# Kernel optimization log

Measured on AMD Instinct MI355X. Metric: run time of the kernel, lower is better.

## Reference

```python
import math
import jax, jax.numpy as jnp
import numpy as np

EMB_DIM, EMB_KS, EMB_HS = 64, 2, 1
H, CS = 4, 32  # n_heads, GLA chunk size
EPS = 1e-5


def _ln4d(x, g, b):
    # LayerNormalization4D: normalize over channel dim (axis 1), biased var
    mu = x.mean(1, keepdims=True)
    var = ((x - mu) ** 2).mean(1, keepdims=True)
    return (x - mu) / jnp.sqrt(var + EPS) * g + b


def _unfold(x):
    # x [N,C,Q] -> [N, L, C*ks]; torch F.unfold feature order is c-major, k-minor
    N, C, Q = x.shape
    L = (Q - EMB_KS) // EMB_HS + 1
    f = jnp.stack([x[:, :, k:k + L] for k in range(EMB_KS)], axis=2)  # [N,C,ks,L]
    return f.reshape(N, C * EMB_KS, L).transpose(0, 2, 1)


def _deconv1d(x, w, b):
    # ConvTranspose1d, stride=EMB_HS=1; x [N,Cin,L], w [Cin,Cout,K]
    N, Cin, L = x.shape
    Cout, K = w.shape[1], w.shape[2]
    out_len = (L - 1) * EMB_HS + K
    y = jnp.zeros((N, Cout, out_len), x.dtype)
    for k in range(K):
        y = y.at[:, :, k:k + L].add(jnp.einsum('ncl,co->nol', x, w[:, :, k]))
    return y + b[None, :, None]


def _gla(x, Wq, Wk, Wv, Wg1, Wg2, Wr, gn, Wo):
    # chunked gated linear attention (use_gk=True, use_gv=False, swish output gate)
    N, L, D = x.shape
    Dk = Wq.shape[1] // H
    Dv = Wv.shape[1] // H
    Lp = -(-L // CS) * CS
    pad = Lp - L
    nc = Lp // CS
    q = (x @ Wq) * (Dk ** -0.5)
    k = x @ Wk
    v = x @ Wv
    gk = jax.nn.log_sigmoid((x @ Wg1) @ Wg2) / 32.0  # gate_logit_normalizer=32

    def chunk(t, dh):
        t = jnp.pad(t, ((0, 0), (0, pad), (0, 0)))
        return t.reshape(N, nc, CS, H, dh)

    q, k, gk, v = chunk(q, Dk), chunk(k, Dk), chunk(gk, Dk), chunk(v, Dv)
    gc = jnp.cumsum(gk, axis=2)                      # within-chunk log-decay [N,nc,CS,H,Dk]
    q_i = q * jnp.exp(gc)
    k_i = k * jnp.exp(-gc)
    mask = jnp.tril(jnp.ones((CS, CS), bool))
    A = jnp.einsum('ncthd,ncshd->nchts', q_i, k_i)   # intra-chunk scores
    A = jnp.where(mask[None, None, None], A, 0.0)
    o_intra = jnp.einsum('nchts,ncshd->ncthd', A, v)
    gl = gc[:, :, -1]                                 # chunk-total log decay [N,nc,H,Dk]
    k_o = k * jnp.exp(gl[:, :, None] - gc)

    def step(S, inp):
        qi, ko, vc, g = inp
        o = jnp.einsum('nthk,nhkv->nthv', qi, S)      # inter-chunk contribution
        S = S * jnp.exp(g)[..., None] + jnp.einsum('nthk,nthv->nhkv', ko, vc)
        return S, o

    S0 = jnp.zeros((N, H, Dk, Dv), x.dtype)
    xs = tuple(jnp.moveaxis(t, 1, 0) for t in (q_i, k_o, v, gl))
    _, o_inter = jax.lax.scan(step, S0, xs)
    o = (o_intra + jnp.moveaxis(o_inter, 0, 1)).reshape(N, Lp, H, Dv)[:, :L]
    # per-head RMSNorm + swish output gate
    o = o / jnp.sqrt(jnp.mean(o * o, -1, keepdims=True) + EPS) * gn.reshape(H, Dv)
    r = x @ Wr
    o = o.reshape(N, L, H * Dv) * (r * jax.nn.sigmoid(r))
    return o @ Wo


def _forward(x, mouth, intra_gamma, intra_beta, intra_Wq, intra_Wk, intra_Wv,
             intra_Wg1, intra_Wg2, intra_Wr, intra_gn, intra_Wo, intra_ct_w, intra_ct_b,
             inter_gamma, inter_beta, inter_Wq, inter_Wk, inter_Wv,
             inter_Wg1, inter_Wg2, inter_Wr, inter_gn, inter_Wo, inter_ct_w, inter_ct_b):
    B, C, old_T, old_Q = x.shape
    T = math.ceil((old_T - EMB_KS) / EMB_HS) * EMB_HS + EMB_KS
    Q = math.ceil((old_Q - EMB_KS) / EMB_HS) * EMB_HS + EMB_KS
    x = jnp.pad(x, ((0, 0), (0, 0), (0, T - old_T), (0, Q - old_Q)))
    # intra (frequency) path
    u = _ln4d(x, intra_gamma, intra_beta)
    u = u.transpose(0, 2, 1, 3).reshape(B * T, C, Q)
    f = _unfold(u)                                    # [B*T, Q-1, C*ks]
    g = _gla(f, intra_Wq, intra_Wk, intra_Wv, intra_Wg1, intra_Wg2, intra_Wr, intra_gn, intra_Wo)
    y = _deconv1d(g.transpose(0, 2, 1), intra_ct_w, intra_ct_b)  # [B*T, C, Q]
    y = y.reshape(B, T, C, Q).transpose(0, 2, 1, 3) + x
    # inter (time) path
    u = _ln4d(y, inter_gamma, inter_beta)
    u = u.transpose(0, 3, 1, 2).reshape(B * Q, C, T)
    f = _unfold(u)                                    # [B*Q, T-1, C*ks]
    g = _gla(f, inter_Wq, inter_Wk, inter_Wv, inter_Wg1, inter_Wg2, inter_Wr, inter_gn, inter_Wo)
    z = _deconv1d(g.transpose(0, 2, 1), inter_ct_w, inter_ct_b)  # [B*Q, C, T]
    z = z.reshape(B, Q, C, T).transpose(0, 2, 3, 1) + y
    return z[..., :old_T, :old_Q]


def setup_inputs() -> dict:
    key = jax.random.key(0)
    ks = jax.random.split(key, 32)
    D = EMB_DIM * EMB_KS       # 128 = GLA d_model
    DKV = 2 * D                # 256 (expand_k = expand_v = 2)

    def w(i, shape, fan):
        return jax.random.normal(ks[i], shape, jnp.float32) / np.sqrt(fan).astype(np.float32)

    inp = {
        'x': jax.random.normal(ks[0], (4, EMB_DIM, 256, 128), jnp.float32),
        'mouth': jax.random.normal(ks[1], (4, 1, 64, 64), jnp.float32),
    }
    for p, base in (('intra', 2), ('inter', 14)):
        inp[p + '_gamma'] = jnp.ones((1, EMB_DIM, 1, 1), jnp.float32)
        inp[p + '_beta'] = jnp.zeros((1, EMB_DIM, 1, 1), jnp.float32)
        inp[p + '_Wq'] = w(base, (D, DKV), D)
        inp[p + '_Wk'] = w(base + 1, (D, DKV), D)
        inp[p + '_Wv'] = w(base + 2, (D, DKV), D)
        inp[p + '_Wg1'] = w(base + 3, (D, 32), D)
        inp[p + '_Wg2'] = w(base + 4, (32, DKV), 32)
        inp[p + '_Wr'] = w(base + 5, (D, DKV), D)
        inp[p + '_gn'] = jnp.ones((DKV,), jnp.float32)
        inp[p + '_Wo'] = w(base + 6, (DKV, D), DKV)
        inp[p + '_ct_w'] = w(base + 7, (D, EMB_DIM, EMB_KS), D * EMB_KS)
        inp[p + '_ct_b'] = jnp.zeros((EMB_DIM,), jnp.float32)
    return inp


def reference(x, mouth, intra_gamma, intra_beta, intra_Wq, intra_Wk, intra_Wv,
              intra_Wg1, intra_Wg2, intra_Wr, intra_gn, intra_Wo, intra_ct_w, intra_ct_b,
              inter_gamma, inter_beta, inter_Wq, inter_Wk, inter_Wv,
              inter_Wg1, inter_Wg2, inter_Wr, inter_gn, inter_Wo, inter_ct_w, inter_ct_b):
    return _forward(x, mouth, intra_gamma, intra_beta, intra_Wq, intra_Wk, intra_Wv,
                    intra_Wg1, intra_Wg2, intra_Wr, intra_gn, intra_Wo, intra_ct_w, intra_ct_b,
                    inter_gamma, inter_beta, inter_Wq, inter_Wk, inter_Wv,
                    inter_Wg1, inter_Wg2, inter_Wr, inter_gn, inter_Wo, inter_ct_w, inter_ct_b)
```

## Files before the change

### kernel.cpp

```cpp
#include <hip/hip_runtime.h>

#define EPS 1e-5f

__device__ __forceinline__ float logsig(float z) {
    return fminf(z, 0.0f) - log1pf(__expf(-fabsf(z)));
}

template<int SLEN, int PSTRIDE>
__global__ __launch_bounds__(512)
__attribute__((amdgpu_waves_per_eu(2, 2)))
void gla_pass(const float* __restrict__ src, float* __restrict__ out,
              const float* __restrict__ gamma, const float* __restrict__ beta,
              const float* __restrict__ Wq, const float* __restrict__ Wk,
              const float* __restrict__ Wv, const float* __restrict__ Wg1,
              const float* __restrict__ Wg2, const float* __restrict__ Wr,
              const float* __restrict__ gn, const float* __restrict__ Wo,
              const float* __restrict__ ctw, const float* __restrict__ ctb)
{
    constexpr int NC = SLEN / 32;
    constexpr int L  = SLEN - 1;

    __shared__ __align__(16) float sxA[64][36];
    __shared__ __align__(16) float sxB[64][36];
    __shared__ __align__(16) float sxr[64][32];
    __shared__ __align__(16) float qf[32][256];
    __shared__ __align__(16) float kf[32][256];
    __shared__ __align__(16) float voc[32][256];
    __shared__ __align__(16) float uni[4608];
    __shared__ __align__(16) float fw1t[32][36];
    __shared__ __align__(16) float gprevs[128];
    __shared__ float egl[256];
    __shared__ float sgam[64], sbet[64];
    __shared__ float smu[33], sinv[33];
    __shared__ float gcarry[256];

    float* const Ats  = uni;
    float* const gdec = uni;

    const int tid  = threadIdx.x;
    const int lane = tid & 63;
    const int wv   = tid >> 6;
    const int h    = wv & 3;
    const int kh   = wv >> 2;
    const int d    = tid & 255;
    const int th   = (tid >> 8) & 1;
    const int n    = blockIdx.x;

    int b, fixedoff;
    if constexpr (PSTRIDE == 1) { b = n >> 8; fixedoff = (n & 255) * 128; }
    else                        { b = n >> 7; fixedoff = (n & 127); }
    const int cbase = (b * 64) * 32768 + fixedoff;

    if (tid < 64)  { sgam[tid] = gamma[tid]; sbet[tid] = beta[tid]; }
    if (tid < 128) gprevs[tid] = 0.0f;

    float S[32];
    #pragma unroll
    for (int k = 0; k < 32; ++k) S[k] = 0.0f;

    const float gnv  = gn[h * 64 + lane];
    const float bias = ctb[lane];

    #pragma unroll
    for (int k = 0; k < 5; ++k) {
        int idx = tid + k * 512;
        if (idx < 64 * 33) {
            int cc = idx / 33, i = idx - cc * 33;
            sxA[cc][i] = src[cbase + cc * 32768 + i * PSTRIDE];
        }
    }

    for (int ch = 0; ch < NC; ++ch) {
        const int l0 = ch * 32;
        float (* const cur)[36] = (ch & 1) ? sxB : sxA;
        float (* const nxt)[36] = (ch & 1) ? sxA : sxB;
        __syncthreads();

        float pre[5];
        const bool pf = (ch + 1 < NC);
        if (pf) {
            const int l0n = l0 + 32;
            #pragma unroll
            for (int k = 0; k < 5; ++k) {
                int idx = tid + k * 512;
                if (idx < 64 * 33) {
                    int cc = idx / 33, i = idx - cc * 33;
                    int p  = l0n + i; if (p > SLEN - 1) p = SLEN - 1;
                    pre[k] = src[cbase + cc * 32768 + p * PSTRIDE];
                }
            }
        }

        for (int col = wv; col < 33; col += 8) {
            float x = cur[lane][col];
            float s1 = x, s2 = x * x;
            #pragma unroll
            for (int off = 32; off > 0; off >>= 1) {
                s1 += __shfl_xor(s1, off, 64);
                s2 += __shfl_xor(s2, off, 64);
            }
            if (lane == 0) {
                float mu  = s1 * (1.0f / 64.0f);
                float var = s2 * (1.0f / 64.0f) - mu * mu;
                smu[col]  = mu;
                sinv[col] = rsqrtf(fmaxf(var, 0.0f) + EPS);
            }
        }
        __syncthreads();

        #pragma unroll
        for (int k = 0; k < 5; ++k) {
            int idx = tid + k * 512;
            if (idx < 64 * 33) {
                int cc = idx / 33, i = idx - cc * 33;
                float x = cur[cc][i];
                if (i < 32) sxr[cc][i] = x;
                cur[cc][i] = (x - smu[i]) * sinv[i] * sgam[cc] + sbet[cc];
            }
        }
        __syncthreads();

        {
            const int m = tid & 31, tg2 = tid >> 5;
            float a0 = 0.0f, a1 = 0.0f;
            for (int cc = 0; cc < 64; ++cc) {
                const float w0 = Wg1[(2*cc)*32 + m], w1 = Wg1[(2*cc+1)*32 + m];
                a0 += cur[cc][tg2]      * w0 + cur[cc][tg2 + 1]  * w1;
                a1 += cur[cc][tg2 + 16] * w0 + cur[cc][tg2 + 17] * w1;
            }
            fw1t[m][tg2] = a0; fw1t[m][tg2 + 16] = a1;
        }
        __syncthreads();

        float erunp[16], erunm[16];
        {
            const int t0 = th * 16;
            float acc2[16];
            #pragma unroll
            for (int t = 0; t < 16; ++t) acc2[t] = 0.0f;
            for (int mm = 0; mm < 32; ++mm) {
                const float w = Wg2[mm * 256 + d];
                #pragma unroll
                for (int i = 0; i < 4; ++i) {
                    float4 f4 = *(const float4*)&fw1t[mm][t0 + 4 * i];
                    acc2[4*i+0] += f4.x * w; acc2[4*i+1] += f4.y * w;
                    acc2[4*i+2] += f4.z * w; acc2[4*i+3] += f4.w * w;
                }
            }
            float r = 0.0f;
            #pragma unroll
            for (int t = 0; t < 16; ++t) {
                if ((l0 + t0 + t) < L) r += logsig(acc2[t]) * (1.0f / 32.0f);
                acc2[t] = r;
            }
            if (th == 0) gcarry[d] = r;
            __syncthreads();
            const float c = (th == 0) ? 0.0f : gcarry[d];
            #pragma unroll
            for (int t = 0; t < 16; ++t) {
                float run = c + acc2[t];
                erunp[t] = __expf(run);
                erunm[t] = __expf(-run);
            }
            if (th == 1) egl[d] = erunp[15];
        }

        if (pf) {
            #pragma unroll
            for (int k = 0; k < 5; ++k) {
                int idx = tid + k * 512;
                if (idx < 64 * 33) {
                    int cc = idx / 33, i = idx - cc * 33;
                    nxt[cc][i] = pre[k];
                }
            }
        }

        {
            const int t0 = th * 16;
            float aq[16], ak[16];
            #pragma unroll
            for (int t = 0; t < 16; ++t) { aq[t] = 0.0f; ak[t] = 0.0f; }
            for (int cc = 0; cc < 64; ++cc) {
                float col[17];
                #pragma unroll
                for (int i = 0; i < 4; ++i) {
                    float4 c4 = *(const float4*)&cur[cc][t0 + 4 * i];
                    col[4*i] = c4.x; col[4*i+1] = c4.y; col[4*i+2] = c4.z; col[4*i+3] = c4.w;
                }
                col[16] = cur[cc][t0 + 16];
                const float wq0 = Wq[(2*cc)*256 + d], wq1 = Wq[(2*cc+1)*256 + d];
                const float wk0 = Wk[(2*cc)*256 + d], wk1 = Wk[(2*cc+1)*256 + d];
                #pragma unroll
                for (int t = 0; t < 16; ++t) {
                    aq[t] += col[t] * wq0 + col[t+1] * wq1;
                    ak[t] += col[t] * wk0 + col[t+1] * wk1;
                }
            }
            #pragma unroll
            for (int t = 0; t < 16; ++t) {
                bool valid = (l0 + t0 + t) < L;
                qf[t0 + t][d] = valid ? aq[t] * 0.125f * erunp[t] : 0.0f;
                kf[t0 + t][d] = valid ? ak[t] * erunm[t] : 0.0f;
            }
        }
        {
            const int t0 = th * 16;
            float av[16];
            #pragma unroll
            for (int t = 0; t < 16; ++t) av[t] = 0.0f;
            for (int cc = 0; cc < 64; ++cc) {
                float col[17];
                #pragma unroll
                for (int i = 0; i < 4; ++i) {
                    float4 c4 = *(const float4*)&cur[cc][t0 + 4 * i];
                    col[4*i] = c4.x; col[4*i+1] = c4.y; col[4*i+2] = c4.z; col[4*i+3] = c4.w;
                }
                col[16] = cur[cc][t0 + 16];
                const float wv0 = Wv[(2*cc)*256 + d], wv1 = Wv[(2*cc+1)*256 + d];
                #pragma unroll
                for (int t = 0; t < 16; ++t) av[t] += col[t] * wv0 + col[t+1] * wv1;
            }
            #pragma unroll
            for (int t = 0; t < 16; ++t)
                voc[t0 + t][d] = ((l0 + t0 + t) < L) ? av[t] : 0.0f;
        }
        __syncthreads();

        const int base = h * 64;
        float vcol[32];
        #pragma unroll
        for (int t = 0; t < 32; ++t) vcol[t] = voc[t][base + lane];

        for (int pi = lane + 64 * kh; pi < 528; pi += 128) {
            float fpi = (float)pi;
            int t = (int)((sqrtf(8.0f * fpi + 1.0f) - 1.0f) * 0.5f);
            if (((t + 1) * (t + 2)) / 2 <= pi) ++t;
            if ((t * (t + 1)) / 2 > pi) --t;
            int s = pi - (t * (t + 1)) / 2;
            float a = 0.0f;
            #pragma unroll
            for (int ii = 0; ii < 16; ++ii) {
                int i = (ii + lane) & 15;
                float4 q4 = *(const float4*)&qf[t][base + 4 * i];
                float4 k4 = *(const float4*)&kf[s][base + 4 * i];
                a += q4.x*k4.x + q4.y*k4.y + q4.z*k4.z + q4.w*k4.w;
            }
            Ats[h * 1152 + t * 36 + s] = a;
        }
        __syncthreads();

        if (kh == 1) {
            #pragma unroll
            for (int t = 0; t < 32; ++t) {
                float oe = 0.0f;
                #pragma unroll
                for (int i = 0; i < 8; ++i) {
                    float4 q4 = *(const float4*)&qf[t][base + 32 + 4 * i];
                    oe += q4.x*S[4*i] + q4.y*S[4*i+1] + q4.z*S[4*i+2] + q4.w*S[4*i+3];
                }
                voc[t][base + lane] = oe;
            }
        }
        __syncthreads();

        if (kh == 0) {
            #pragma unroll
            for (int t = 0; t < 32; ++t) {
                float ot = voc[t][base + lane];
                #pragma unroll
                for (int i = 0; i < 8; ++i) {
                    float4 q4 = *(const float4*)&qf[t][base + 4 * i];
                    ot += q4.x*S[4*i] + q4.y*S[4*i+1] + q4.z*S[4*i+2] + q4.w*S[4*i+3];
                }
                const float* arow = &Ats[h * 1152 + t * 36];
                #pragma unroll
                for (int s4 = 0; s4 + 4 <= t + 1; s4 += 4) {
                    float4 a4 = *(const float4*)&arow[s4];
                    ot += a4.x*vcol[s4] + a4.y*vcol[s4+1] + a4.z*vcol[s4+2] + a4.w*vcol[s4+3];
                }
                #pragma unroll
                for (int s = (t + 1) & ~3; s <= t; ++s) ot += arow[s] * vcol[s];
                float ss = ot * ot;
                #pragma unroll
                for (int off = 32; off > 0; off >>= 1) ss += __shfl_xor(ss, off, 64);
                voc[t][base + lane] = ot * rsqrtf(ss * (1.0f / 64.0f) + EPS) * gnv;
            }
        } else {
            const int kb = base + 32;
            #pragma unroll
            for (int i = 0; i < 8; ++i) {
                float s0 = 0.0f, s1 = 0.0f, s2 = 0.0f, s3 = 0.0f;
                #pragma unroll
                for (int t = 0; t < 32; ++t) {
                    float4 k4 = *(const float4*)&kf[t][kb + 4 * i];
                    const float vt = vcol[t];
                    s0 += k4.x * vt; s1 += k4.y * vt; s2 += k4.z * vt; s3 += k4.w * vt;
                }
                S[4*i+0] = egl[kb + 4*i+0] * (S[4*i+0] + s0);
                S[4*i+1] = egl[kb + 4*i+1] * (S[4*i+1] + s1);
                S[4*i+2] = egl[kb + 4*i+2] * (S[4*i+2] + s2);
                S[4*i+3] = egl[kb + 4*i+3] * (S[4*i+3] + s3);
            }
        }
        __syncthreads();

        if (kh == 0) {
            const int kb = base;
            #pragma unroll
            for (int i = 0; i < 8; ++i) {
                float s0 = 0.0f, s1 = 0.0f, s2 = 0.0f, s3 = 0.0f;
                #pragma unroll
                for (int t = 0; t < 32; ++t) {
                    float4 k4 = *(const float4*)&kf[t][kb + 4 * i];
                    const float vt = vcol[t];
                    s0 += k4.x * vt; s1 += k4.y * vt; s2 += k4.z * vt; s3 += k4.w * vt;
                }
                S[4*i+0] = egl[kb + 4*i+0] * (S[4*i+0] + s0);
                S[4*i+1] = egl[kb + 4*i+1] * (S[4*i+1] + s1);
                S[4*i+2] = egl[kb + 4*i+2] * (S[4*i+2] + s2);
                S[4*i+3] = egl[kb + 4*i+3] * (S[4*i+3] + s3);
            }
        }

        {
            const int t0 = th * 16;
            float ar[16];
            #pragma unroll
            for (int t = 0; t < 16; ++t) ar[t] = 0.0f;
            for (int cc = 0; cc < 64; ++cc) {
                float col[17];
                #pragma unroll
                for (int i = 0; i < 4; ++i) {
                    float4 c4 = *(const float4*)&cur[cc][t0 + 4 * i];
                    col[4*i] = c4.x; col[4*i+1] = c4.y; col[4*i+2] = c4.z; col[4*i+3] = c4.w;
                }
                col[16] = cur[cc][t0 + 16];
                const float w0 = Wr[(2*cc)*256 + d], w1 = Wr[(2*cc+1)*256 + d];
                #pragma unroll
                for (int t = 0; t < 16; ++t) ar[t] += col[t] * w0 + col[t+1] * w1;
            }
            #pragma unroll
            for (int t = 0; t < 16; ++t) {
                const float r = ar[t];
                voc[t0 + t][d] *= r / (1.0f + __expf(-r));
            }
        }
        __syncthreads();

        {
            const int m2  = tid & 63;
            const int tg4 = tid >> 6;
            float accA[4] = {0,0,0,0}, accB[4] = {0,0,0,0};
            for (int j = 0; j < 256; j += 4) {
                float wA0 = Wo[(j+0)*128 + m2],      wB0 = Wo[(j+0)*128 + m2 + 64];
                float wA1 = Wo[(j+1)*128 + m2],      wB1 = Wo[(j+1)*128 + m2 + 64];
                float wA2 = Wo[(j+2)*128 + m2],      wB2 = Wo[(j+2)*128 + m2 + 64];
                float wA3 = Wo[(j+3)*128 + m2],      wB3 = Wo[(j+3)*128 + m2 + 64];
                #pragma unroll
                for (int i = 0; i < 4; ++i) {
                    float4 o4 = *(const float4*)&voc[tg4 * 4 + i][j];
                    accA[i] += o4.x*wA0 + o4.y*wA1 + o4.z*wA2 + o4.w*wA3;
                    accB[i] += o4.x*wB0 + o4.y*wB1 + o4.z*wB2 + o4.w*wB3;
                }
            }
            #pragma unroll
            for (int i = 0; i < 4; ++i) {
                gdec[(tg4 * 4 + i) * 132 + m2]      = accA[i];
                gdec[(tg4 * 4 + i) * 132 + m2 + 64] = accB[i];
            }
        }
        __syncthreads();

        {
            const int o  = lane;
            const int pg = wv;
            const float2* ctw2 = (const float2*)ctw;
            float acc4[4] = {0,0,0,0};
            for (int c4 = 0; c4 < 128; c4 += 4) {
                float2 w0 = ctw2[(c4+0)*64 + o];
                float2 w1 = ctw2[(c4+1)*64 + o];
                float2 w2 = ctw2[(c4+2)*64 + o];
                float2 w3 = ctw2[(c4+3)*64 + o];
                float4 r[5];
                r[0] = (pg == 0) ? *(const float4*)&gprevs[c4]
                                 : *(const float4*)&gdec[(pg*4 - 1) * 132 + c4];
                #pragma unroll
                for (int j = 0; j < 4; ++j)
                    r[j+1] = *(const float4*)&gdec[(pg*4 + j) * 132 + c4];
                #pragma unroll
                for (int i = 0; i < 4; ++i) {
                    acc4[i] += r[i+1].x*w0.x + r[i].x*w0.y
                             + r[i+1].y*w1.x + r[i].y*w1.y
                             + r[i+1].z*w2.x + r[i].z*w2.y
                             + r[i+1].w*w3.x + r[i].w*w3.y;
                }
            }
            #pragma unroll
            for (int i = 0; i < 4; ++i) {
                const int tl = pg * 4 + i;
                const int oi = cbase + o * 32768 + (l0 + tl) * PSTRIDE;
                out[oi] = acc4[i] + bias + sxr[o][tl];
            }
        }
        __syncthreads();
        if (tid < 128) gprevs[tid] = gdec[31 * 132 + tid];
    }
}

extern "C" void kernel_launch(void* const* d_in, const int* in_sizes, int n_in,
                              void* d_out, int out_size, void* d_ws, size_t ws_size,
                              hipStream_t stream)
{
    const float* x = (const float*)d_in[0];
    float* y = (float*)d_ws;
    float* z = (float*)d_out;

    gla_pass<128, 1><<<dim3(1024), dim3(512), 0, stream>>>(
        x, y,
        (const float*)d_in[2],  (const float*)d_in[3],  (const float*)d_in[4],
        (const float*)d_in[5],  (const float*)d_in[6],  (const float*)d_in[7],
        (const float*)d_in[8],  (const float*)d_in[9],  (const float*)d_in[10],
        (const float*)d_in[11], (const float*)d_in[12], (const float*)d_in[13]);

    gla_pass<256, 128><<<dim3(512), dim3(512), 0, stream>>>(
        y, z,
        (const float*)d_in[14], (const float*)d_in[15], (const float*)d_in[16],
        (const float*)d_in[17], (const float*)d_in[18], (const float*)d_in[19],
        (const float*)d_in[20], (const float*)d_in[21], (const float*)d_in[22],
        (const float*)d_in[23], (const float*)d_in[24], (const float*)d_in[25]);
}
```

Before: 5.909 ms.

## Pack projection weights into interleaved float4 layout and prefetch per iteration

Adds a small pre-kernel that repacks Wq/Wk, Wv/Wr and Wg1 into interleaved float4/float2 arrays in workspace, so each projection loop loads one vector per channel pair instead of four scalar loads, and software-prefetches the next iteration's weights. It also recomputes exp gates on the fly instead of holding 32 registers of exponentials to reduce register pressure, and halves the LayerNorm shuffle reduction by having each half-wave handle a column. Costs an extra launch plus workspace traffic each call, and Wv/Wr loads now fetch unused halves.

```diff
diff --git a/kernel.cpp b/kernel.cpp
--- a/kernel.cpp
+++ b/kernel.cpp
@@ -4,6 +4,43 @@
 
 __device__ __forceinline__ float logsig(float z) {
     return fminf(z, 0.0f) - log1pf(__expf(-fabsf(z)));
+}
+
+__global__ __launch_bounds__(256)
+void pack_weights(const float* __restrict__ Wq0, const float* __restrict__ Wk0,
+                  const float* __restrict__ Wv0, const float* __restrict__ Wr0,
+                  const float* __restrict__ Wg10,
+                  const float* __restrict__ Wq1, const float* __restrict__ Wk1,
+                  const float* __restrict__ Wv1, const float* __restrict__ Wr1,
+                  const float* __restrict__ Wg11,
+                  float* __restrict__ pk)
+{
+    int idx = blockIdx.x * 256 + threadIdx.x;
+    int p   = (idx >= 34816) ? 1 : 0;
+    int j   = idx - p * 34816;
+    const float* Wq  = p ? Wq1  : Wq0;
+    const float* Wk  = p ? Wk1  : Wk0;
+    const float* Wv  = p ? Wv1  : Wv0;
+    const float* Wr  = p ? Wr1  : Wr0;
+    const float* Wg1 = p ? Wg11 : Wg10;
+    float* base = pk + p * 135168;
+    if (j < 16384) {
+        int cc = j >> 8, d = j & 255;
+        float4 v = { Wq[(2*cc)*256 + d], Wq[(2*cc+1)*256 + d],
+                     Wk[(2*cc)*256 + d], Wk[(2*cc+1)*256 + d] };
+        ((float4*)base)[j] = v;
+    } else if (j < 32768) {
+        int jj = j - 16384;
+        int cc = jj >> 8, d = jj & 255;
+        float4 v = { Wv[(2*cc)*256 + d], Wv[(2*cc+1)*256 + d],
+                     Wr[(2*cc)*256 + d], Wr[(2*cc+1)*256 + d] };
+        ((float4*)(base + 65536))[jj] = v;
+    } else {
+        int jj = j - 32768;
+        int cc = jj >> 5, m = jj & 31;
+        float2 v = { Wg1[(2*cc)*32 + m], Wg1[(2*cc+1)*32 + m] };
+        ((float2*)(base + 131072))[jj] = v;
+    }
 }
 
 template<int SLEN, int PSTRIDE>
@@ -11,9 +48,9 @@
 __attribute__((amdgpu_waves_per_eu(2, 2)))
 void gla_pass(const float* __restrict__ src, float* __restrict__ out,
               const float* __restrict__ gamma, const float* __restrict__ beta,
-              const float* __restrict__ Wq, const float* __restrict__ Wk,
-              const float* __restrict__ Wv, const float* __restrict__ Wg1,
-              const float* __restrict__ Wg2, const float* __restrict__ Wr,
+              const float4* __restrict__ pWqk, const float4* __restrict__ pWvr,
+              const float2* __restrict__ pWg1,
+              const float* __restrict__ Wg2,
               const float* __restrict__ gn, const float* __restrict__ Wo,
               const float* __restrict__ ctw, const float* __restrict__ ctb)
 {
@@ -91,15 +128,20 @@
             }
         }
 
-        for (int col = wv; col < 33; col += 8) {
-            float x = cur[lane][col];
-            float s1 = x, s2 = x * x;
-            #pragma unroll
-            for (int off = 32; off > 0; off >>= 1) {
+        for (int cp = wv; cp < 17; cp += 8) {
+            const int col = 2 * cp + (lane >> 5);
+            float s1 = 0.0f, s2 = 0.0f;
+            if (col < 33) {
+                const int c0 = (lane & 31) * 2;
+                float x0 = cur[c0][col], x1 = cur[c0 + 1][col];
+                s1 = x0 + x1; s2 = x0 * x0 + x1 * x1;
+            }
+            #pragma unroll
+            for (int off = 16; off > 0; off >>= 1) {
                 s1 += __shfl_xor(s1, off, 64);
                 s2 += __shfl_xor(s2, off, 64);
             }
-            if (lane == 0) {
+            if ((lane & 31) == 0 && col < 33) {
                 float mu  = s1 * (1.0f / 64.0f);
                 float var = s2 * (1.0f / 64.0f) - mu * mu;
                 smu[col]  = mu;
@@ -123,16 +165,19 @@
         {
             const int m = tid & 31, tg2 = tid >> 5;
             float a0 = 0.0f, a1 = 0.0f;
+            float2 wg = pWg1[m];
+            #pragma unroll 2
             for (int cc = 0; cc < 64; ++cc) {
-                const float w0 = Wg1[(2*cc)*32 + m], w1 = Wg1[(2*cc+1)*32 + m];
-                a0 += cur[cc][tg2]      * w0 + cur[cc][tg2 + 1]  * w1;
-                a1 += cur[cc][tg2 + 16] * w0 + cur[cc][tg2 + 17] * w1;
+                float2 wn = pWg1[((cc + 1) & 63) * 32 + m];
+                a0 += cur[cc][tg2]      * wg.x + cur[cc][tg2 + 1]  * wg.y;
+                a1 += cur[cc][tg2 + 16] * wg.x + cur[cc][tg2 + 17] * wg.y;
+                wg = wn;
             }
             fw1t[m][tg2] = a0; fw1t[m][tg2 + 16] = a1;
         }
         __syncthreads();
 
-        float erunp[16], erunm[16];
+        float rn[16];
         {
             const int t0 = th * 16;
             float acc2[16];
@@ -157,12 +202,8 @@
             __syncthreads();
             const float c = (th == 0) ? 0.0f : gcarry[d];
             #pragma unroll
-            for (int t = 0; t < 16; ++t) {
-                float run = c + acc2[t];
-                erunp[t] = __expf(run);
-                erunm[t] = __expf(-run);
-            }
-            if (th == 1) egl[d] = erunp[15];
+            for (int t = 0; t < 16; ++t) rn[t] = c + acc2[t];
+            if (th == 1) egl[d] = __expf(rn[15]);
         }
 
         if (pf) {
@@ -181,7 +222,9 @@
             float aq[16], ak[16];
             #pragma unroll
             for (int t = 0; t < 16; ++t) { aq[t] = 0.0f; ak[t] = 0.0f; }
+            float4 w = pWqk[d];
             for (int cc = 0; cc < 64; ++cc) {
+                float4 wn = pWqk[((cc + 1) & 63) * 256 + d];
                 float col[17];
                 #pragma unroll
                 for (int i = 0; i < 4; ++i) {
@@ -189,19 +232,18 @@
                     col[4*i] = c4.x; col[4*i+1] = c4.y; col[4*i+2] = c4.z; col[4*i+3] = c4.w;
                 }
                 col[16] = cur[cc][t0 + 16];
-                const float wq0 = Wq[(2*cc)*256 + d], wq1 = Wq[(2*cc+1)*256 + d];
-                const float wk0 = Wk[(2*cc)*256 + d], wk1 = Wk[(2*cc+1)*256 + d];
                 #pragma unroll
                 for (int t = 0; t < 16; ++t) {
-                    aq[t] += col[t] * wq0 + col[t+1] * wq1;
-                    ak[t] += col[t] * wk0 + col[t+1] * wk1;
-                }
+                    aq[t] += col[t] * w.x + col[t+1] * w.y;
+                    ak[t] += col[t] * w.z + col[t+1] * w.w;
+                }
+                w = wn;
             }
             #pragma unroll
             for (int t = 0; t < 16; ++t) {
                 bool valid = (l0 + t0 + t) < L;
-                qf[t0 + t][d] = valid ? aq[t] * 0.125f * erunp[t] : 0.0f;
-                kf[t0 + t][d] = valid ? ak[t] * erunm[t] : 0.0f;
+                qf[t0 + t][d] = valid ? aq[t] * 0.125f * __expf(rn[t]) : 0.0f;
+                kf[t0 + t][d] = valid ? ak[t] * __expf(-rn[t]) : 0.0f;
             }
         }
         {
@@ -209,7 +251,9 @@
             float av[16];
             #pragma unroll
             for (int t = 0; t < 16; ++t) av[t] = 0.0f;
+            float4 w = pWvr[d];
             for (int cc = 0; cc < 64; ++cc) {
+                float4 wn = pWvr[((cc + 1) & 63) * 256 + d];
                 float col[17];
                 #pragma unroll
                 for (int i = 0; i < 4; ++i) {
@@ -217,9 +261,9 @@
                     col[4*i] = c4.x; col[4*i+1] = c4.y; col[4*i+2] = c4.z; col[4*i+3] = c4.w;
                 }
                 col[16] = cur[cc][t0 + 16];
-                const float wv0 = Wv[(2*cc)*256 + d], wv1 = Wv[(2*cc+1)*256 + d];
-                #pragma unroll
-                for (int t = 0; t < 16; ++t) av[t] += col[t] * wv0 + col[t+1] * wv1;
+                #pragma unroll
+                for (int t = 0; t < 16; ++t) av[t] += col[t] * w.x + col[t+1] * w.y;
+                w = wn;
             }
             #pragma unroll
             for (int t = 0; t < 16; ++t)
@@ -328,7 +372,9 @@
             float ar[16];
             #pragma unroll
             for (int t = 0; t < 16; ++t) ar[t] = 0.0f;
+            float4 w = pWvr[d];
             for (int cc = 0; cc < 64; ++cc) {
+                float4 wn = pWvr[((cc + 1) & 63) * 256 + d];
                 float col[17];
                 #pragma unroll
                 for (int i = 0; i < 4; ++i) {
@@ -336,9 +382,9 @@
                     col[4*i] = c4.x; col[4*i+1] = c4.y; col[4*i+2] = c4.z; col[4*i+3] = c4.w;
                 }
                 col[16] = cur[cc][t0 + 16];
-                const float w0 = Wr[(2*cc)*256 + d], w1 = Wr[(2*cc+1)*256 + d];
-                #pragma unroll
-                for (int t = 0; t < 16; ++t) ar[t] += col[t] * w0 + col[t+1] * w1;
+                #pragma unroll
+                for (int t = 0; t < 16; ++t) ar[t] += col[t] * w.z + col[t+1] * w.w;
+                w = wn;
             }
             #pragma unroll
             for (int t = 0; t < 16; ++t) {
@@ -413,20 +459,31 @@
                               hipStream_t stream)
 {
     const float* x = (const float*)d_in[0];
-    float* y = (float*)d_ws;
-    float* z = (float*)d_out;
+    float* y  = (float*)d_ws;
+    float* pk = (float*)d_ws + 8388608;
+    float* z  = (float*)d_out;
+
+    pack_weights<<<dim3(272), dim3(256), 0, stream>>>(
+        (const float*)d_in[4],  (const float*)d_in[5],  (const float*)d_in[6],
+        (const float*)d_in[9],  (const float*)d_in[7],
+        (const float*)d_in[16], (const float*)d_in[17], (const float*)d_in[18],
+        (const float*)d_in[21], (const float*)d_in[19],
+        pk);
 
     gla_pass<128, 1><<<dim3(1024), dim3(512), 0, stream>>>(
         x, y,
-        (const float*)d_in[2],  (const float*)d_in[3],  (const float*)d_in[4],
-        (const float*)d_in[5],  (const float*)d_in[6],  (const float*)d_in[7],
-        (const float*)d_in[8],  (const float*)d_in[9],  (const float*)d_in[10],
-        (const float*)d_in[11], (const float*)d_in[12], (const float*)d_in[13]);
+        (const float*)d_in[2],  (const float*)d_in[3],
+        (const float4*)pk, (const float4*)(pk + 65536), (const float2*)(pk + 131072),
+        (const float*)d_in[8],
+        (const float*)d_in[10], (const float*)d_in[11],
+        (const float*)d_in[12], (const float*)d_in[13]);
 
     gla_pass<256, 128><<<dim3(512), dim3(512), 0, stream>>>(
         y, z,
-        (const float*)d_in[14], (const float*)d_in[15], (const float*)d_in[16],
-        (const float*)d_in[17], (const float*)d_in[18], (const float*)d_in[19],
-        (const float*)d_in[20], (const float*)d_in[21], (const float*)d_in[22],
-        (const float*)d_in[23], (const float*)d_in[24], (const float*)d_in[25]);
+        (const float*)d_in[14], (const float*)d_in[15],
+        (const float4*)(pk + 135168), (const float4*)(pk + 135168 + 65536),
+        (const float2*)(pk + 135168 + 131072),
+        (const float*)d_in[20],
+        (const float*)d_in[22], (const float*)d_in[23],
+        (const float*)d_in[24], (const float*)d_in[25]);
 }
```

Result: no change. 5.953 ms (+0.7%).

## Store q/k/v intermediates in fp16 LDS and shrink shared memory footprint

Applied to the files above, without the earlier changes.

Stores the per-chunk q, k and v/output buffers in LDS as fp16 instead of fp32, and uses packed fp16 dot products (fdot2) for the intra-chunk score computation. The double-buffered input tile and residual buffer are removed: the next chunk is written into a single buffer after compute, and the residual is re-read from global memory. The forced waves-per-eu attribute is dropped. Together these cut LDS usage so more blocks can be resident per CU and LDS bandwidth drops. The cost is reduced precision in attention intermediates and extra global reads for the residual.

```diff
diff --git a/kernel.cpp b/kernel.cpp
--- a/kernel.cpp
+++ b/kernel.cpp
@@ -1,14 +1,29 @@
 #include <hip/hip_runtime.h>
 
 #define EPS 1e-5f
+
+typedef _Float16 half_t;
+typedef _Float16 h2_t __attribute__((ext_vector_type(2)));
+union U16 { uint4 u; h2_t h[4]; };
 
 __device__ __forceinline__ float logsig(float z) {
     return fminf(z, 0.0f) - log1pf(__expf(-fabsf(z)));
 }
 
+__device__ __forceinline__ float hdot2(h2_t a, h2_t b, float c) {
+#if defined(__has_builtin)
+#if __has_builtin(__builtin_amdgcn_fdot2)
+    return __builtin_amdgcn_fdot2(a, b, c, false);
+#else
+    return c + (float)a[0] * (float)b[0] + (float)a[1] * (float)b[1];
+#endif
+#else
+    return c + (float)a[0] * (float)b[0] + (float)a[1] * (float)b[1];
+#endif
+}
+
 template<int SLEN, int PSTRIDE>
 __global__ __launch_bounds__(512)
-__attribute__((amdgpu_waves_per_eu(2, 2)))
 void gla_pass(const float* __restrict__ src, float* __restrict__ out,
               const float* __restrict__ gamma, const float* __restrict__ beta,
               const float* __restrict__ Wq, const float* __restrict__ Wk,
@@ -20,20 +35,18 @@
     constexpr int NC = SLEN / 32;
     constexpr int L  = SLEN - 1;
 
-    __shared__ __align__(16) float sxA[64][36];
-    __shared__ __align__(16) float sxB[64][36];
-    __shared__ __align__(16) float sxr[64][32];
-    __shared__ __align__(16) float qf[32][256];
-    __shared__ __align__(16) float kf[32][256];
-    __shared__ __align__(16) float voc[32][256];
-    __shared__ __align__(16) float uni[4608];
-    __shared__ __align__(16) float fw1t[32][36];
-    __shared__ __align__(16) float gprevs[128];
+    __shared__ __align__(16) float  sx[64][36];
+    __shared__ __align__(16) half_t qsh[32][256];
+    __shared__ __align__(16) half_t ksh[32][256];
+    __shared__ __align__(16) half_t vsh[32][256];
+    __shared__ __align__(16) float  uni[4608];
+    __shared__ __align__(16) float  gprevs[128];
     __shared__ float egl[256];
     __shared__ float sgam[64], sbet[64];
     __shared__ float smu[33], sinv[33];
     __shared__ float gcarry[256];
 
+    float* const fw1t = uni;
     float* const Ats  = uni;
     float* const gdec = uni;
 
@@ -66,14 +79,12 @@
         int idx = tid + k * 512;
         if (idx < 64 * 33) {
             int cc = idx / 33, i = idx - cc * 33;
-            sxA[cc][i] = src[cbase + cc * 32768 + i * PSTRIDE];
+            sx[cc][i] = src[cbase + cc * 32768 + i * PSTRIDE];
         }
     }
 
     for (int ch = 0; ch < NC; ++ch) {
         const int l0 = ch * 32;
-        float (* const cur)[36] = (ch & 1) ? sxB : sxA;
-        float (* const nxt)[36] = (ch & 1) ? sxA : sxB;
         __syncthreads();
 
         float pre[5];
@@ -92,7 +103,7 @@
         }
 
         for (int col = wv; col < 33; col += 8) {
-            float x = cur[lane][col];
+            float x = sx[lane][col];
             float s1 = x, s2 = x * x;
             #pragma unroll
             for (int off = 32; off > 0; off >>= 1) {
@@ -113,9 +124,7 @@
             int idx = tid + k * 512;
             if (idx < 64 * 33) {
                 int cc = idx / 33, i = idx - cc * 33;
-                float x = cur[cc][i];
-                if (i < 32) sxr[cc][i] = x;
-                cur[cc][i] = (x - smu[i]) * sinv[i] * sgam[cc] + sbet[cc];
+                sx[cc][i] = (sx[cc][i] - smu[i]) * sinv[i] * sgam[cc] + sbet[cc];
             }
         }
         __syncthreads();
@@ -125,14 +134,14 @@
             float a0 = 0.0f, a1 = 0.0f;
             for (int cc = 0; cc < 64; ++cc) {
                 const float w0 = Wg1[(2*cc)*32 + m], w1 = Wg1[(2*cc+1)*32 + m];
-                a0 += cur[cc][tg2]      * w0 + cur[cc][tg2 + 1]  * w1;
-                a1 += cur[cc][tg2 + 16] * w0 + cur[cc][tg2 + 17] * w1;
-            }
-            fw1t[m][tg2] = a0; fw1t[m][tg2 + 16] = a1;
-        }
-        __syncthreads();
-
-        float erunp[16], erunm[16];
+                a0 += sx[cc][tg2]      * w0 + sx[cc][tg2 + 1]  * w1;
+                a1 += sx[cc][tg2 + 16] * w0 + sx[cc][tg2 + 17] * w1;
+            }
+            fw1t[m * 36 + tg2] = a0; fw1t[m * 36 + tg2 + 16] = a1;
+        }
+        __syncthreads();
+
+        float rn[16];
         {
             const int t0 = th * 16;
             float acc2[16];
@@ -142,7 +151,7 @@
                 const float w = Wg2[mm * 256 + d];
                 #pragma unroll
                 for (int i = 0; i < 4; ++i) {
-                    float4 f4 = *(const float4*)&fw1t[mm][t0 + 4 * i];
+                    float4 f4 = *(const float4*)&fw1t[mm * 36 + t0 + 4 * i];
                     acc2[4*i+0] += f4.x * w; acc2[4*i+1] += f4.y * w;
                     acc2[4*i+2] += f4.z * w; acc2[4*i+3] += f4.w * w;
                 }
@@ -157,23 +166,8 @@
             __syncthreads();
             const float c = (th == 0) ? 0.0f : gcarry[d];
             #pragma unroll
-            for (int t = 0; t < 16; ++t) {
-                float run = c + acc2[t];
-                erunp[t] = __expf(run);
-                erunm[t] = __expf(-run);
-            }
-            if (th == 1) egl[d] = erunp[15];
-        }
-
-        if (pf) {
-            #pragma unroll
-            for (int k = 0; k < 5; ++k) {
-                int idx = tid + k * 512;
-                if (idx < 64 * 33) {
-                    int cc = idx / 33, i = idx - cc * 33;
-                    nxt[cc][i] = pre[k];
-                }
-            }
+            for (int t = 0; t < 16; ++t) rn[t] = c + acc2[t];
+            if (th == 1) egl[d] = __expf(rn[15]);
         }
 
         {
@@ -185,10 +179,10 @@
                 float col[17];
                 #pragma unroll
                 for (int i = 0; i < 4; ++i) {
-                    float4 c4 = *(const float4*)&cur[cc][t0 + 4 * i];
+                    float4 c4 = *(const float4*)&sx[cc][t0 + 4 * i];
                     col[4*i] = c4.x; col[4*i+1] = c4.y; col[4*i+2] = c4.z; col[4*i+3] = c4.w;
                 }
-                col[16] = cur[cc][t0 + 16];
+                col[16] = sx[cc][t0 + 16];
                 const float wq0 = Wq[(2*cc)*256 + d], wq1 = Wq[(2*cc+1)*256 + d];
                 const float wk0 = Wk[(2*cc)*256 + d], wk1 = Wk[(2*cc+1)*256 + d];
                 #pragma unroll
@@ -200,8 +194,8 @@
             #pragma unroll
             for (int t = 0; t < 16; ++t) {
                 bool valid = (l0 + t0 + t) < L;
-                qf[t0 + t][d] = valid ? aq[t] * 0.125f * erunp[t] : 0.0f;
-                kf[t0 + t][d] = valid ? ak[t] * erunm[t] : 0.0f;
+                qsh[t0 + t][d] = (half_t)(valid ? aq[t] * 0.125f * __expf(rn[t]) : 0.0f);
+                ksh[t0 + t][d] = (half_t)(valid ? ak[t] * __expf(-rn[t]) : 0.0f);
             }
         }
         {
@@ -213,24 +207,24 @@
                 float col[17];
                 #pragma unroll
                 for (int i = 0; i < 4; ++i) {
-                    float4 c4 = *(const float4*)&cur[cc][t0 + 4 * i];
+                    float4 c4 = *(const float4*)&sx[cc][t0 + 4 * i];
                     col[4*i] = c4.x; col[4*i+1] = c4.y; col[4*i+2] = c4.z; col[4*i+3] = c4.w;
                 }
-                col[16] = cur[cc][t0 + 16];
+                col[16] = sx[cc][t0 + 16];
                 const float wv0 = Wv[(2*cc)*256 + d], wv1 = Wv[(2*cc+1)*256 + d];
                 #pragma unroll
                 for (int t = 0; t < 16; ++t) av[t] += col[t] * wv0 + col[t+1] * wv1;
             }
             #pragma unroll
             for (int t = 0; t < 16; ++t)
-                voc[t0 + t][d] = ((l0 + t0 + t) < L) ? av[t] : 0.0f;
+                vsh[t0 + t][d] = (half_t)(((l0 + t0 + t) < L) ? av[t] : 0.0f);
         }
         __syncthreads();
 
         const int base = h * 64;
         float vcol[32];
         #pragma unroll
-        for (int t = 0; t < 32; ++t) vcol[t] = voc[t][base + lane];
+        for (int t = 0; t < 32; ++t) vcol[t] = (float)vsh[t][base + lane];
 
         for (int pi = lane + 64 * kh; pi < 528; pi += 128) {
             float fpi = (float)pi;
@@ -238,13 +232,15 @@
             if (((t + 1) * (t + 2)) / 2 <= pi) ++t;
             if ((t * (t + 1)) / 2 > pi) --t;
             int s = pi - (t * (t + 1)) / 2;
+            const uint4* q16 = (const uint4*)&qsh[t][base];
+            const uint4* k16 = (const uint4*)&ksh[s][base];
             float a = 0.0f;
             #pragma unroll
-            for (int ii = 0; ii < 16; ++ii) {
-                int i = (ii + lane) & 15;
-                float4 q4 = *(const float4*)&qf[t][base + 4 * i];
-                float4 k4 = *(const float4*)&kf[s][base + 4 * i];
-                a += q4.x*k4.x + q4.y*k4.y + q4.z*k4.z + q4.w*k4.w;
+            for (int ii = 0; ii < 8; ++ii) {
+                int i = (ii + lane) & 7;
+                U16 qa, ka; qa.u = q16[i]; ka.u = k16[i];
+                #pragma unroll
+                for (int j = 0; j < 4; ++j) a = hdot2(qa.h[j], ka.h[j], a);
             }
             Ats[h * 1152 + t * 36 + s] = a;
         }
@@ -253,13 +249,18 @@
         if (kh == 1) {
             #pragma unroll
             for (int t = 0; t < 32; ++t) {
+                const uint4* qp = (const uint4*)&qsh[t][base + 32];
                 float oe = 0.0f;
                 #pragma unroll
-                for (int i = 0; i < 8; ++i) {
-                    float4 q4 = *(const float4*)&qf[t][base + 32 + 4 * i];
-                    oe += q4.x*S[4*i] + q4.y*S[4*i+1] + q4.z*S[4*i+2] + q4.w*S[4*i+3];
-                }
-                voc[t][base + lane] = oe;
+                for (int i = 0; i < 4; ++i) {
+                    U16 u; u.u = qp[i];
+                    #pragma unroll
+                    for (int j = 0; j < 4; ++j) {
+                        oe += (float)u.h[j][0] * S[i*8 + 2*j]
+                            + (float)u.h[j][1] * S[i*8 + 2*j + 1];
+                    }
+                }
+                vsh[t][base + lane] = (half_t)oe;
             }
         }
         __syncthreads();
@@ -267,11 +268,16 @@
         if (kh == 0) {
             #pragma unroll
             for (int t = 0; t < 32; ++t) {
-                float ot = voc[t][base + lane];
-                #pragma unroll
-                for (int i = 0; i < 8; ++i) {
-                    float4 q4 = *(const float4*)&qf[t][base + 4 * i];
-                    ot += q4.x*S[4*i] + q4.y*S[4*i+1] + q4.z*S[4*i+2] + q4.w*S[4*i+3];
+                float ot = (float)vsh[t][base + lane];
+                const uint4* qp = (const uint4*)&qsh[t][base];
+                #pragma unroll
+                for (int i = 0; i < 4; ++i) {
+                    U16 u; u.u = qp[i];
+                    #pragma unroll
+                    for (int j = 0; j < 4; ++j) {
+                        ot += (float)u.h[j][0] * S[i*8 + 2*j]
+                            + (float)u.h[j][1] * S[i*8 + 2*j + 1];
+                    }
                 }
                 const float* arow = &Ats[h * 1152 + t * 36];
                 #pragma unroll
@@ -284,23 +290,26 @@
                 float ss = ot * ot;
                 #pragma unroll
                 for (int off = 32; off > 0; off >>= 1) ss += __shfl_xor(ss, off, 64);
-                voc[t][base + lane] = ot * rsqrtf(ss * (1.0f / 64.0f) + EPS) * gnv;
+                vsh[t][base + lane] = (half_t)(ot * rsqrtf(ss * (1.0f / 64.0f) + EPS) * gnv);
             }
         } else {
             const int kb = base + 32;
             #pragma unroll
-            for (int i = 0; i < 8; ++i) {
-                float s0 = 0.0f, s1 = 0.0f, s2 = 0.0f, s3 = 0.0f;
+            for (int i = 0; i < 4; ++i) {
+                float s8[8] = {0,0,0,0,0,0,0,0};
                 #pragma unroll
                 for (int t = 0; t < 32; ++t) {
-                    float4 k4 = *(const float4*)&kf[t][kb + 4 * i];
+                    U16 u; u.u = *(const uint4*)&ksh[t][kb + 8*i];
                     const float vt = vcol[t];
-                    s0 += k4.x * vt; s1 += k4.y * vt; s2 += k4.z * vt; s3 += k4.w * vt;
-                }
-                S[4*i+0] = egl[kb + 4*i+0] * (S[4*i+0] + s0);
-                S[4*i+1] = egl[kb + 4*i+1] * (S[4*i+1] + s1);
-                S[4*i+2] = egl[kb + 4*i+2] * (S[4*i+2] + s2);
-                S[4*i+3] = egl[kb + 4*i+3] * (S[4*i+3] + s3);
+                    #pragma unroll
+                    for (int j = 0; j < 4; ++j) {
+                        s8[2*j]   += (float)u.h[j][0] * vt;
+                        s8[2*j+1] += (float)u.h[j][1] * vt;
+                    }
+                }
+                #pragma unroll
+                for (int j = 0; j < 8; ++j)
+                    S[8*i+j] = egl[kb + 8*i + j] * (S[8*i+j] + s8[j]);
             }
         }
         __syncthreads();
@@ -308,18 +317,21 @@
         if (kh == 0) {
             const int kb = base;
             #pragma unroll
-            for (int i = 0; i < 8; ++i) {
-                float s0 = 0.0f, s1 = 0.0f, s2 = 0.0f, s3 = 0.0f;
+            for (int i = 0; i < 4; ++i) {
+                float s8[8] = {0,0,0,0,0,0,0,0};
                 #pragma unroll
                 for (int t = 0; t < 32; ++t) {
-                    float4 k4 = *(const float4*)&kf[t][kb + 4 * i];
+                    U16 u; u.u = *(const uint4*)&ksh[t][kb + 8*i];
                     const float vt = vcol[t];
-                    s0 += k4.x * vt; s1 += k4.y * vt; s2 += k4.z * vt; s3 += k4.w * vt;
-                }
-                S[4*i+0] = egl[kb + 4*i+0] * (S[4*i+0] + s0);
-                S[4*i+1] = egl[kb + 4*i+1] * (S[4*i+1] + s1);
-                S[4*i+2] = egl[kb + 4*i+2] * (S[4*i+2] + s2);
-                S[4*i+3] = egl[kb + 4*i+3] * (S[4*i+3] + s3);
+                    #pragma unroll
+                    for (int j = 0; j < 4; ++j) {
+                        s8[2*j]   += (float)u.h[j][0] * vt;
+                        s8[2*j+1] += (float)u.h[j][1] * vt;
+                    }
+                }
+                #pragma unroll
+                for (int j = 0; j < 8; ++j)
+                    S[8*i+j] = egl[kb + 8*i + j] * (S[8*i+j] + s8[j]);
             }
         }
 
@@ -332,36 +344,58 @@
                 float col[17];
                 #pragma unroll
                 for (int i = 0; i < 4; ++i) {
-                    float4 c4 = *(const float4*)&cur[cc][t0 + 4 * i];
+                    float4 c4 = *(const float4*)&sx[cc][t0 + 4 * i];
                     col[4*i] = c4.x; col[4*i+1] = c4.y; col[4*i+2] = c4.z; col[4*i+3] = c4.w;
                 }
-                col[16] = cur[cc][t0 + 16];
+                col[16] = sx[cc][t0 + 16];
                 const float w0 = Wr[(2*cc)*256 + d], w1 = Wr[(2*cc+1)*256 + d];
                 #pragma unroll
                 for (int t = 0; t < 16; ++t) ar[t] += col[t] * w0 + col[t+1] * w1;
             }
             #pragma unroll
             for (int t = 0; t < 16; ++t) {
-                const float r = ar[t];
-                voc[t0 + t][d] *= r / (1.0f + __expf(-r));
-            }
-        }
-        __syncthreads();
+                const float r  = ar[t];
+                const float ov = (float)vsh[t0 + t][d];
+                vsh[t0 + t][d] = (half_t)(ov * r / (1.0f + __expf(-r)));
+            }
+        }
+        __syncthreads();
+
+        if (pf) {
+            #pragma unroll
+            for (int k = 0; k < 5; ++k) {
+                int idx = tid + k * 512;
+                if (idx < 64 * 33) {
+                    int cc = idx / 33, i = idx - cc * 33;
+                    sx[cc][i] = pre[k];
+                }
+            }
+        }
+        float resid[4];
+        #pragma unroll
+        for (int i = 0; i < 4; ++i)
+            resid[i] = src[cbase + lane * 32768 + (l0 + wv * 4 + i) * PSTRIDE];
 
         {
             const int m2  = tid & 63;
             const int tg4 = tid >> 6;
             float accA[4] = {0,0,0,0}, accB[4] = {0,0,0,0};
-            for (int j = 0; j < 256; j += 4) {
-                float wA0 = Wo[(j+0)*128 + m2],      wB0 = Wo[(j+0)*128 + m2 + 64];
-                float wA1 = Wo[(j+1)*128 + m2],      wB1 = Wo[(j+1)*128 + m2 + 64];
-                float wA2 = Wo[(j+2)*128 + m2],      wB2 = Wo[(j+2)*128 + m2 + 64];
-                float wA3 = Wo[(j+3)*128 + m2],      wB3 = Wo[(j+3)*128 + m2 + 64];
-                #pragma unroll
-                for (int i = 0; i < 4; ++i) {
-                    float4 o4 = *(const float4*)&voc[tg4 * 4 + i][j];
-                    accA[i] += o4.x*wA0 + o4.y*wA1 + o4.z*wA2 + o4.w*wA3;
-                    accB[i] += o4.x*wB0 + o4.y*wB1 + o4.z*wB2 + o4.w*wB3;
+            for (int jb = 0; jb < 32; ++jb) {
+                float wA[8], wB[8];
+                #pragma unroll
+                for (int u2 = 0; u2 < 8; ++u2) {
+                    wA[u2] = Wo[(8*jb + u2)*128 + m2];
+                    wB[u2] = Wo[(8*jb + u2)*128 + m2 + 64];
+                }
+                #pragma unroll
+                for (int i = 0; i < 4; ++i) {
+                    U16 u; u.u = *(const uint4*)&vsh[tg4 * 4 + i][8 * jb];
+                    #pragma unroll
+                    for (int j = 0; j < 4; ++j) {
+                        float o0 = (float)u.h[j][0], o1 = (float)u.h[j][1];
+                        accA[i] += o0 * wA[2*j] + o1 * wA[2*j+1];
+                        accB[i] += o0 * wB[2*j] + o1 * wB[2*j+1];
+                    }
                 }
             }
             #pragma unroll
@@ -400,7 +434,7 @@
             for (int i = 0; i < 4; ++i) {
                 const int tl = pg * 4 + i;
                 const int oi = cbase + o * 32768 + (l0 + tl) * PSTRIDE;
-                out[oi] = acc4[i] + bias + sxr[o][tl];
+                out[oi] = acc4[i] + bias + resid[i];
             }
         }
         __syncthreads();
```

New measurement: 7.399 ms. 25.2% more time.
